# Kernel optimization log

Hardware: AMD Instinct MI355X
Metric: run time of the kernel (lower is better)

Reference implementation:

```python
import jax, jax.numpy as jnp
import numpy as np

K = 3  # kernel size


def _qparams(t):
    # dynamic per-tensor affine quant params: scale=(max-min)/255, zero=-round(min/scale)
    mx = jnp.max(t)
    mn = jnp.min(t)
    s = (mx - mn) / 255.0
    z = -jnp.round(mn / s)
    return s, z


def _quant(t, s, z):
    return jnp.clip(jnp.round(t / s + z), 0.0, 255.0).astype(jnp.int32)


def setup_inputs() -> dict:
    key = jax.random.key(0)
    k1, k2, k3 = jax.random.split(key, 3)
    x = jax.random.normal(k1, (4, 32, 34, 34), dtype=jnp.float32)
    weight = jax.random.normal(k2, (64, 32, K, K), dtype=jnp.float32) * 0.1
    bias = jax.random.normal(k3, (64,), dtype=jnp.float32) * 0.1
    a = jnp.arange(256, dtype=jnp.float32)
    lut = a[:, None] * a[None, :]
    return {"x": x, "weight": weight, "lut": lut, "bias": bias}


def reference(x, weight, lut, bias):
    OC = weight.shape[0]
    # --- dynamic per-tensor quantization of activations and weights ---
    s_x, z_x = _qparams(x)
    s_w, z_w = _qparams(weight)
    qx = _quant(x, s_x, z_x)                       # [B, C, H, W] uint8 codes (int32)
    qw = _quant(weight, s_w, z_w).reshape(OC, -1)  # [OC, C*K*K]

    # --- im2col on the quantized activations (VALID, stride 1) ---
    patches = jax.lax.conv_general_dilated_patches(
        qx.astype(jnp.float32), (K, K), (1, 1), 'VALID')  # [B, C*K*K, OH, OW]
    B, CKK, OH, OW = patches.shape
    qxp = patches.astype(jnp.int32).transpose(0, 2, 3, 1).reshape(B, OH * OW, CKK)

    # --- LUT-based approximate multiply-accumulate ---
    # idx[b, p, oc, k] = qxp[b, p, k] * 256 + qw[oc, k]
    idx = qxp[:, :, None, :] * 256 + qw[None, None, :, :]          # [B, P, OC, CKK]
    acc = jnp.take(lut.reshape(-1), idx).sum(axis=-1)              # [B, P, OC]

    # --- affine dequantization of the integer accumulator ---
    sum_qw = qw.sum(axis=-1).astype(jnp.float32)                   # [OC]
    sum_qx = qxp.sum(axis=-1).astype(jnp.float32)                  # [B, P]
    out = s_x * s_w * (acc
                       - z_x * sum_qw[None, None, :]
                       - z_w * sum_qx[:, :, None]
                       + CKK * z_x * z_w)                          # [B, P, OC]
    out = out.reshape(B, OH, OW, OC).transpose(0, 3, 1, 2)         # [B, OC, OH, OW]
    return out + bias[None, :, None, None]
```

## Files before the change

kernel.cpp:

```cpp
#include <hip/hip_runtime.h>
#include <stdint.h>

#define B_    4
#define C_    32
#define HW_   34
#define OC_   64
#define CKK_  288

#define NX (B_*C_*HW_*HW_)
#define NW (OC_*C_*9)
#define NX4 (NX/4)
#define NW4 (NW/4)
#define NT4 (NX4+NW4)

__device__ __forceinline__ unsigned fmap(float f) {
  int i = __float_as_int(f);
  return (i < 0) ? ~(unsigned)i : ((unsigned)i | 0x80000000u);
}
__device__ __forceinline__ float funmap(unsigned u) {
  int i = (u & 0x80000000u) ? (int)(u ^ 0x80000000u) : ~(int)u;
  return __int_as_float(i);
}
__device__ __forceinline__ unsigned umax_(unsigned a, unsigned b){ return a>b?a:b; }
__device__ __forceinline__ unsigned umin_(unsigned a, unsigned b){ return a<b?a:b; }

__device__ __forceinline__ unsigned dot4(unsigned a, unsigned b, unsigned acc) {
#if __has_builtin(__builtin_amdgcn_udot4)
  return __builtin_amdgcn_udot4(a, b, acc, false);
#else
  acc += (a & 0xFFu) * (b & 0xFFu);
  acc += ((a >> 8) & 0xFFu) * ((b >> 8) & 0xFFu);
  acc += ((a >> 16) & 0xFFu) * ((b >> 16) & 0xFFu);
  acc += (a >> 24) * (b >> 24);
  return acc;
#endif
}

__global__ __launch_bounds__(256) void minmax_kernel(const float* __restrict__ x,
                                                     const float* __restrict__ w,
                                                     unsigned* __restrict__ ws) {
  unsigned xmax = 0, xnmin = 0, wmax = 0, wnmin = 0;
  int tid = blockIdx.x * 256 + threadIdx.x;
  int stride = gridDim.x * 256;
  for (int u = tid; u < NT4; u += stride) {
    bool isx = u < NX4;
    float4 v = isx ? ((const float4*)x)[u] : ((const float4*)w)[u - NX4];
    unsigned m0 = fmap(v.x), m1 = fmap(v.y), m2 = fmap(v.z), m3 = fmap(v.w);
    unsigned hi = umax_(umax_(m0, m1), umax_(m2, m3));
    unsigned lo = ~umin_(umin_(m0, m1), umin_(m2, m3));
    if (isx) { xmax = umax_(xmax, hi); xnmin = umax_(xnmin, lo); }
    else     { wmax = umax_(wmax, hi); wnmin = umax_(wnmin, lo); }
  }
  for (int m = 32; m; m >>= 1) {
    xmax  = umax_(xmax,  (unsigned)__shfl_xor((int)xmax,  m, 64));
    xnmin = umax_(xnmin, (unsigned)__shfl_xor((int)xnmin, m, 64));
    wmax  = umax_(wmax,  (unsigned)__shfl_xor((int)wmax,  m, 64));
    wnmin = umax_(wnmin, (unsigned)__shfl_xor((int)wnmin, m, 64));
  }
  __shared__ unsigned red[4][4];
  int wid = threadIdx.x >> 6, lane = threadIdx.x & 63;
  if (lane == 0) { red[wid][0] = xmax; red[wid][1] = xnmin; red[wid][2] = wmax; red[wid][3] = wnmin; }
  __syncthreads();
  if (threadIdx.x < 4) {
    unsigned v = umax_(umax_(red[0][threadIdx.x], red[1][threadIdx.x]),
                       umax_(red[2][threadIdx.x], red[3][threadIdx.x]));
    atomicMax(&ws[threadIdx.x], v);
  }
}

__global__ __launch_bounds__(256) void conv_kernel(const float* __restrict__ x,
                                                   const float* __restrict__ w,
                                                   const float* __restrict__ bias,
                                                   const unsigned* __restrict__ ws,
                                                   float* __restrict__ out) {
  const int och = blockIdx.x;
  const int oh  = blockIdx.y;
  const int b   = blockIdx.z;
  const int t   = threadIdx.x;

  const float mxx = funmap(ws[0]), mnx = funmap(~ws[1]);
  const float mxw = funmap(ws[2]), mnw = funmap(~ws[3]);
  const float s_x = (mxx - mnx) / 255.0f;
  const float z_x = -rintf(mnx / s_x);
  const float s_w = (mxw - mnw) / 255.0f;
  const float z_w = -rintf(mnw / s_w);

  __shared__ unsigned s_qw[32 * 32 * 4];
  __shared__ unsigned s_pt[32 * 32 * 4];
  __shared__ int s_sumqw[32];

  for (int i = t; i < 32 * 32 * 4; i += 256) { s_qw[i] = 0; s_pt[i] = 0; }
  __syncthreads();

  {
    const float* wsrc = w + och * (32 * CKK_);
    unsigned char* qb = (unsigned char*)s_qw;
    #pragma unroll
    for (int i = 0; i < 36; i++) {
      int idx = t + i * 256;
      float v = wsrc[idx] / s_w + z_w;
      int q = (int)rintf(v);
      q = min(max(q, 0), 255);
      int ocl = idx / CKK_;
      int k   = idx - ocl * CKK_;
      int c   = k / 9;
      int kr  = k - c * 9;
      int r   = kr / 3;
      int kw  = kr - r * 3;
      qb[(ocl * 32 + (c ^ ((ocl >> 1) & 7))) * 16 + r * 4 + kw] = (unsigned char)q;
    }
  }
  {
    const float* xsrc = x + (size_t)b * (C_ * HW_ * HW_);
    unsigned char* pb = (unsigned char*)s_pt;
    #pragma unroll
    for (int i = 0; i < 13; i++) {
      int idx = t + i * 256;
      if (idx < 32 * 3 * HW_) {
        int c   = idx / (3 * HW_);
        int rem = idx - c * (3 * HW_);
        int r   = rem / HW_;
        int wc  = rem - r * HW_;
        float v = xsrc[(c * HW_ + (oh + r)) * HW_ + wc] / s_x + z_x;
        int q = (int)rintf(v);
        q = min(max(q, 0), 255);
        #pragma unroll
        for (int kw = 0; kw < 3; kw++) {
          int ow = wc - kw;
          if (0 <= ow && ow < 32)
            pb[(ow * 32 + (c ^ ((ow >> 1) & 7))) * 16 + r * 4 + kw] = (unsigned char)q;
        }
      }
    }
  }
  __syncthreads();

  if (t < 32) {
    unsigned s = 0;
    const unsigned* row = s_qw + t * 128;
    for (int i = 0; i < 128; i++) s = dot4(row[i], 0x01010101u, s);
    s_sumqw[t] = (int)s;
  }

  const int owp = t & 15, ocp = t >> 4;
  const int ow0 = owp * 2, oc0 = ocp * 2;
  const unsigned psw = (unsigned)(owp & 7);
  const unsigned wsw = (unsigned)(ocp & 7);

  unsigned a00 = 0, a01 = 0, a10 = 0, a11 = 0, sx0 = 0, sx1 = 0;
  const uint4* qw4 = (const uint4*)s_qw;
  const uint4* pt4 = (const uint4*)s_pt;
  #pragma unroll 8
  for (int c = 0; c < 32; c++) {
    uint4 w0 = qw4[oc0 * 32 + (c ^ wsw)];
    uint4 w1 = qw4[(oc0 + 1) * 32 + (c ^ wsw)];
    uint4 p0 = pt4[ow0 * 32 + (c ^ psw)];
    uint4 p1 = pt4[(ow0 + 1) * 32 + (c ^ psw)];
    a00 = dot4(p0.x, w0.x, a00); a00 = dot4(p0.y, w0.y, a00); a00 = dot4(p0.z, w0.z, a00);
    a01 = dot4(p0.x, w1.x, a01); a01 = dot4(p0.y, w1.y, a01); a01 = dot4(p0.z, w1.z, a01);
    a10 = dot4(p1.x, w0.x, a10); a10 = dot4(p1.y, w0.y, a10); a10 = dot4(p1.z, w0.z, a10);
    a11 = dot4(p1.x, w1.x, a11); a11 = dot4(p1.y, w1.y, a11); a11 = dot4(p1.z, w1.z, a11);
    sx0 = dot4(p0.x, 0x01010101u, sx0); sx0 = dot4(p0.y, 0x01010101u, sx0); sx0 = dot4(p0.z, 0x01010101u, sx0);
    sx1 = dot4(p1.x, 0x01010101u, sx1); sx1 = dot4(p1.y, 0x01010101u, sx1); sx1 = dot4(p1.z, 0x01010101u, sx1);
  }
  __syncthreads();

  const float sxw = s_x * s_w;
  const float zz  = 288.0f * z_x * z_w;
  const int ocg0 = och * 32 + oc0;
  const float bz0 = bias[ocg0], bz1 = bias[ocg0 + 1];
  const float sqw0 = (float)s_sumqw[oc0], sqw1 = (float)s_sumqw[oc0 + 1];
  const float fs0 = (float)(int)sx0, fs1 = (float)(int)sx1;

  float2 r0, r1;
  r0.x = sxw * ((float)(int)a00 - z_x * sqw0 - z_w * fs0 + zz) + bz0;
  r0.y = sxw * ((float)(int)a10 - z_x * sqw0 - z_w * fs1 + zz) + bz0;
  r1.x = sxw * ((float)(int)a01 - z_x * sqw1 - z_w * fs0 + zz) + bz1;
  r1.y = sxw * ((float)(int)a11 - z_x * sqw1 - z_w * fs1 + zz) + bz1;

  float* obase = out + ((((size_t)b * OC_ + ocg0) * 32 + oh) * 32 + ow0);
  *(float2*)obase = r0;
  *(float2*)(obase + 32 * 32) = r1;
}

extern "C" void kernel_launch(void* const* d_in, const int* in_sizes, int n_in,
                              void* d_out, int out_size, void* d_ws, size_t ws_size,
                              hipStream_t stream) {
  const float* x    = (const float*)d_in[0];
  const float* w    = (const float*)d_in[1];
  const float* bias = (const float*)d_in[3];
  unsigned* ws = (unsigned*)d_ws;

  hipMemsetAsync(d_ws, 0, 16, stream);
  minmax_kernel<<<64, 256, 0, stream>>>(x, w, ws);
  dim3 grid(2, 32, 4);
  conv_kernel<<<grid, 256, 0, stream>>>(x, w, bias, ws, (float*)d_out);
}
```

Before: 76.61 us.

## Fuse minmax and conv into one cooperative kernel with a grid sync

Merges the min/max reduction kernel and the conv kernel into a single cooperative launch of 256 blocks. The first 64 blocks write per-block partial min/max values to workspace, a grid-wide sync follows, and then every block reduces the 64 partials itself before doing its conv tile. This removes the memset and one kernel launch boundary. In exchange it adds the cost of a cooperative launch and grid barrier, plus a redundant partial reduction in every block. The shared-memory zeroing is also vectorised to uint4 stores.

```diff
diff --git a/kernel.cpp b/kernel.cpp
--- a/kernel.cpp
+++ b/kernel.cpp
@@ -1,5 +1,8 @@
 #include <hip/hip_runtime.h>
+#include <hip/hip_cooperative_groups.h>
 #include <stdint.h>
+
+namespace cg = cooperative_groups;
 
 #define B_    4
 #define C_    32
@@ -36,60 +39,79 @@
 #endif
 }
 
-__global__ __launch_bounds__(256) void minmax_kernel(const float* __restrict__ x,
-                                                     const float* __restrict__ w,
-                                                     unsigned* __restrict__ ws) {
-  unsigned xmax = 0, xnmin = 0, wmax = 0, wnmin = 0;
-  int tid = blockIdx.x * 256 + threadIdx.x;
-  int stride = gridDim.x * 256;
-  for (int u = tid; u < NT4; u += stride) {
-    bool isx = u < NX4;
-    float4 v = isx ? ((const float4*)x)[u] : ((const float4*)w)[u - NX4];
-    unsigned m0 = fmap(v.x), m1 = fmap(v.y), m2 = fmap(v.z), m3 = fmap(v.w);
-    unsigned hi = umax_(umax_(m0, m1), umax_(m2, m3));
-    unsigned lo = ~umin_(umin_(m0, m1), umin_(m2, m3));
-    if (isx) { xmax = umax_(xmax, hi); xnmin = umax_(xnmin, lo); }
-    else     { wmax = umax_(wmax, hi); wnmin = umax_(wnmin, lo); }
-  }
-  for (int m = 32; m; m >>= 1) {
-    xmax  = umax_(xmax,  (unsigned)__shfl_xor((int)xmax,  m, 64));
-    xnmin = umax_(xnmin, (unsigned)__shfl_xor((int)xnmin, m, 64));
-    wmax  = umax_(wmax,  (unsigned)__shfl_xor((int)wmax,  m, 64));
-    wnmin = umax_(wnmin, (unsigned)__shfl_xor((int)wnmin, m, 64));
-  }
-  __shared__ unsigned red[4][4];
-  int wid = threadIdx.x >> 6, lane = threadIdx.x & 63;
-  if (lane == 0) { red[wid][0] = xmax; red[wid][1] = xnmin; red[wid][2] = wmax; red[wid][3] = wnmin; }
-  __syncthreads();
-  if (threadIdx.x < 4) {
-    unsigned v = umax_(umax_(red[0][threadIdx.x], red[1][threadIdx.x]),
-                       umax_(red[2][threadIdx.x], red[3][threadIdx.x]));
-    atomicMax(&ws[threadIdx.x], v);
-  }
-}
-
-__global__ __launch_bounds__(256) void conv_kernel(const float* __restrict__ x,
-                                                   const float* __restrict__ w,
-                                                   const float* __restrict__ bias,
-                                                   const unsigned* __restrict__ ws,
-                                                   float* __restrict__ out) {
-  const int och = blockIdx.x;
-  const int oh  = blockIdx.y;
-  const int b   = blockIdx.z;
+__global__ __launch_bounds__(256) void fused_kernel(const float* __restrict__ x,
+                                                    const float* __restrict__ w,
+                                                    const float* __restrict__ bias,
+                                                    unsigned* __restrict__ ws,
+                                                    float* __restrict__ out) {
+  const int bid = blockIdx.x;
   const int t   = threadIdx.x;
-
-  const float mxx = funmap(ws[0]), mnx = funmap(~ws[1]);
-  const float mxw = funmap(ws[2]), mnw = funmap(~ws[3]);
+  const int wid = t >> 6, lane = t & 63;
+
+  __shared__ unsigned red1[4][4];
+  __shared__ unsigned red2[16];
+  __shared__ unsigned s_qw[32 * 32 * 4];
+  __shared__ unsigned s_pt[32 * 32 * 4];
+  __shared__ int s_sumqw[32];
+
+  if (bid < 64) {
+    unsigned xmax = 0, xnmin = 0, wmax = 0, wnmin = 0;
+    for (int u = bid * 256 + t; u < NT4; u += 64 * 256) {
+      bool isx = u < NX4;
+      float4 v = isx ? ((const float4*)x)[u] : ((const float4*)w)[u - NX4];
+      unsigned m0 = fmap(v.x), m1 = fmap(v.y), m2 = fmap(v.z), m3 = fmap(v.w);
+      unsigned hi = umax_(umax_(m0, m1), umax_(m2, m3));
+      unsigned lo = ~umin_(umin_(m0, m1), umin_(m2, m3));
+      if (isx) { xmax = umax_(xmax, hi); xnmin = umax_(xnmin, lo); }
+      else     { wmax = umax_(wmax, hi); wnmin = umax_(wnmin, lo); }
+    }
+    for (int m = 32; m; m >>= 1) {
+      xmax  = umax_(xmax,  (unsigned)__shfl_xor((int)xmax,  m, 64));
+      xnmin = umax_(xnmin, (unsigned)__shfl_xor((int)xnmin, m, 64));
+      wmax  = umax_(wmax,  (unsigned)__shfl_xor((int)wmax,  m, 64));
+      wnmin = umax_(wnmin, (unsigned)__shfl_xor((int)wnmin, m, 64));
+    }
+    if (lane == 0) { red1[wid][0] = xmax; red1[wid][1] = xnmin; red1[wid][2] = wmax; red1[wid][3] = wnmin; }
+    __syncthreads();
+    if (t < 4) {
+      unsigned v = umax_(umax_(red1[0][t], red1[1][t]), umax_(red1[2][t], red1[3][t]));
+      ws[bid * 4 + t] = v;
+    }
+  }
+
+  cg::this_grid().sync();
+
+  {
+    unsigned v = ws[t];
+    v = umax_(v, (unsigned)__shfl_xor((int)v,  4, 64));
+    v = umax_(v, (unsigned)__shfl_xor((int)v,  8, 64));
+    v = umax_(v, (unsigned)__shfl_xor((int)v, 16, 64));
+    v = umax_(v, (unsigned)__shfl_xor((int)v, 32, 64));
+    if (lane < 4) red2[wid * 4 + lane] = v;
+    __syncthreads();
+  }
+  const unsigned uxmax  = umax_(umax_(red2[0], red2[4]), umax_(red2[ 8], red2[12]));
+  const unsigned uxnmin = umax_(umax_(red2[1], red2[5]), umax_(red2[ 9], red2[13]));
+  const unsigned uwmax  = umax_(umax_(red2[2], red2[6]), umax_(red2[10], red2[14]));
+  const unsigned uwnmin = umax_(umax_(red2[3], red2[7]), umax_(red2[11], red2[15]));
+
+  const float mxx = funmap(uxmax), mnx = funmap(~uxnmin);
+  const float mxw = funmap(uwmax), mnw = funmap(~uwnmin);
   const float s_x = (mxx - mnx) / 255.0f;
   const float z_x = -rintf(mnx / s_x);
   const float s_w = (mxw - mnw) / 255.0f;
   const float z_w = -rintf(mnw / s_w);
 
-  __shared__ unsigned s_qw[32 * 32 * 4];
-  __shared__ unsigned s_pt[32 * 32 * 4];
-  __shared__ int s_sumqw[32];
-
-  for (int i = t; i < 32 * 32 * 4; i += 256) { s_qw[i] = 0; s_pt[i] = 0; }
+  const int och = bid & 1;
+  const int oh  = (bid >> 1) & 31;
+  const int b   = bid >> 6;
+
+  {
+    const uint4 z4 = make_uint4(0, 0, 0, 0);
+    uint4* q4 = (uint4*)s_qw; uint4* p4 = (uint4*)s_pt;
+    #pragma unroll
+    for (int i = 0; i < 4; i++) { q4[t + i * 256] = z4; p4[t + i * 256] = z4; }
+  }
   __syncthreads();
 
   {
@@ -189,10 +211,9 @@
   const float* x    = (const float*)d_in[0];
   const float* w    = (const float*)d_in[1];
   const float* bias = (const float*)d_in[3];
-  unsigned* ws = (unsigned*)d_ws;
-
-  hipMemsetAsync(d_ws, 0, 16, stream);
-  minmax_kernel<<<64, 256, 0, stream>>>(x, w, ws);
-  dim3 grid(2, 32, 4);
-  conv_kernel<<<grid, 256, 0, stream>>>(x, w, bias, ws, (float*)d_out);
-}
+  unsigned* ws      = (unsigned*)d_ws;
+  float* out        = (float*)d_out;
+
+  void* args[] = { (void*)&x, (void*)&w, (void*)&bias, (void*)&ws, (void*)&out };
+  hipLaunchCooperativeKernel((void*)fused_kernel, dim3(256), dim3(256), args, 0, stream);
+}
```

After: 112.9 us. 47.3% more time.
